# Optimization experiments

Measured on AMD Instinct MI355X. Metric: run time of the kernel, lower is better.

## Reference

```python
import jax, jax.numpy as jnp
import numpy as np

MS = [1, 2, 4, 8, 16]          # args.ms_token_size
RESI = 0.5                     # Phi resi_ratio
# PhiPartiallyShared: 4 phis, ticks = linspace(1/(2*4)... wait K==4 -> linspace(1/3/K, 1-1/3/K, K)
_TICKS = np.linspace(1.0 / 3.0 / 4.0, 1.0 - 1.0 / 3.0 / 4.0, 4)
PHI_IDX = [int(np.argmin(np.abs(_TICKS - (si / (len(MS) - 1))))) for si in range(len(MS))]


def _phi(h, w, b):
    # Phi.forward: h*(1-r) + conv3x3(h)*r
    c = jax.lax.conv_general_dilated(h, w, (1, 1), 'SAME',
                                     dimension_numbers=('NCHW', 'OIHW', 'NCHW'))
    c = c + b[None, :, None, None]
    return h * (1.0 - RESI) + c * RESI


def _area_down(z, ph, pw):
    # F.interpolate mode='area' with integer ratio == block mean
    B, C, H, W = z.shape
    return z.reshape(B, C, ph, H // ph, pw, W // pw).mean(axis=(3, 5))


def setup_inputs() -> dict:
    key = jax.random.key(0)
    k1, k2, k3 = jax.random.split(key, 3)
    B, C, H, W = 32, 64, 16, 16
    K = 8192
    f = jax.random.normal(k1, (B, C, H, W), dtype=jnp.float32)
    # nn.Embedding init: uniform(-1/K, 1/K)
    emb_w = jax.random.uniform(k2, (K, C), dtype=jnp.float32,
                               minval=-1.0 / K, maxval=1.0 / K)
    phi_w = jax.random.normal(k3, (4, C, C, 3, 3), dtype=jnp.float32) * 0.02
    phi_b = jnp.zeros((4, C), dtype=jnp.float32)
    return {'f': f, 'emb_w': emb_w, 'phi_w': phi_w, 'phi_b': phi_b}


def reference(f, emb_w, phi_w, phi_b):
    B, C, H, W = f.shape
    f = jax.lax.stop_gradient(f)  # z_enc.detach()
    z_rest = f
    f_hat = jnp.zeros_like(f)
    w_sq = jnp.sum(emb_w * emb_w, axis=1)  # [K]
    for si, pn in enumerate(MS):
        last = (si == len(MS) - 1)
        z = z_rest if last else _area_down(z_rest, pn, pn)
        zf = z.transpose(0, 2, 3, 1).reshape(-1, C)  # [B*pn*pn, C]
        # ||z||^2 + ||w||^2 - 2 z.w  (matches square-sum + addmm)
        d = jnp.sum(zf * zf, axis=1, keepdims=True) + w_sq[None, :] \
            - 2.0 * (zf @ emb_w.T)
        tok = jnp.argmin(d, axis=1)                  # [B*pn*pn]
        h = emb_w[tok].reshape(B, pn, pn, C).transpose(0, 3, 1, 2)
        if not last:
            h = jax.image.resize(h, (B, C, H, W), method='cubic')
        h = _phi(h, phi_w[PHI_IDX[si]], phi_b[PHI_IDX[si]])
        f_hat = f_hat + h
        z_rest = z_rest - h
    return f_hat
```

## Files before the change

### kernel.cpp

```cpp
#include <hip/hip_runtime.h>
#include <math.h>
#include <float.h>

#define BB 32
#define CC 64
#define KK 8192
#define NPIX 256
#define NELEM (BB*CC*NPIX)

typedef unsigned short u16;
typedef __attribute__((ext_vector_type(8))) short bf16x8;
typedef __attribute__((ext_vector_type(4))) float f32x4;

__device__ __forceinline__ u16 f2bf(float v) {
  unsigned u = __float_as_uint(v);
  return (u16)((u + 0x7FFFu + ((u >> 16) & 1u)) >> 16);
}

__global__ void k_prep(const float* __restrict__ f, float* __restrict__ zr,
                       float* __restrict__ out, const float* __restrict__ emb,
                       float* __restrict__ wsq32, u16* __restrict__ ehi) {
  int i = blockIdx.x * 256 + threadIdx.x;
  if (i < NELEM) { zr[i] = f[i]; out[i] = 0.f; ehi[i] = f2bf(emb[i]); }
  if (i < KK) {
    const float* row = emb + i * 64;
    double s = 0.0;
    #pragma unroll
    for (int c = 0; c < 64; ++c) s += (double)row[c] * (double)row[c];
    wsq32[i] = (float)s;
  }
}

__global__ void k_down(const float* __restrict__ zr, float* __restrict__ zd, int pn) {
#pragma clang fp contract(off)
  int i = blockIdx.x * 256 + threadIdx.x;
  int pnpn = pn * pn;
  int n = BB * CC * pnpn;
  if (i >= n) return;
  int x = i % pn; int y = (i / pn) % pn; int bc = i / pnpn;
  int bs = 16 / pn;
  const float* src = zr + bc * NPIX + (y * bs) * 16 + x * bs;
  float acc = 0.f;
  for (int dy = 0; dy < bs; ++dy) {
    const float* a = src + dy * 16;
    float s;
    if (bs == 16) {
      float r[8];
      #pragma unroll
      for (int j = 0; j < 8; ++j) r[j] = a[j] + a[8 + j];
      s = ((r[0] + r[1]) + (r[2] + r[3])) + ((r[4] + r[5]) + (r[6] + r[7]));
    } else if (bs == 8) {
      s = ((a[0] + a[1]) + (a[2] + a[3])) + ((a[4] + a[5]) + (a[6] + a[7]));
    } else if (bs == 4) {
      s = ((a[0] + a[1]) + a[2]) + a[3];
    } else {
      s = a[0] + a[1];
    }
    acc = acc + s;
  }
  zd[i] = acc * (1.f / (bs * bs));
}

__global__ __launch_bounds__(256) void k_pack(
    const float* __restrict__ zr, int pn, int bs,
    u16* __restrict__ zhi, float* __restrict__ zt32, float* __restrict__ zsq32) {
#pragma clang fp contract(off)
  int tid = threadIdx.x;
  int lv = tid >> 6, c = tid & 63;
  int vec = blockIdx.x * 4 + lv;
  int pnpn = pn * pn;
  int b = vec / pnpn, p = vec % pnpn;
  int y = p / pn, x = p % pn;
  const float* src = zr + ((size_t)(b * 64 + c)) * 256 + (y * bs) * 16 + x * bs;
  float v;
  if (bs == 1) {
    v = src[0];
  } else {
    v = (src[0] + src[1]) + (src[16] + src[17]);
    v = v * 0.25f;
  }
  zhi[(size_t)vec * 64 + c] = f2bf(v);
  zt32[(size_t)vec * 64 + c] = v;
  double sq = (double)v * (double)v;
  #pragma unroll
  for (int m = 1; m < 64; m <<= 1)
    sq += __shfl_xor(sq, m, 64);
  if (c == 0) zsq32[vec] = (float)sq;
}

__global__ __launch_bounds__(256, 4) void k_argmin(
    const float* __restrict__ zd, const float* __restrict__ emb,
    const float* __restrict__ wsq32,
    float* __restrict__ pd, int* __restrict__ pi,
    int numVec, int pnpn, int kchunk) {
#pragma clang fp contract(off)
  __shared__ __align__(16) float zt[32][68];
  __shared__ __align__(16) float et[64 * 64];
  __shared__ float ws_s[64];
  __shared__ float red_d[256];
  __shared__ int   red_i[256];
  int tid = threadIdx.x;
  int v0 = blockIdx.x * 32;
  int kbase = blockIdx.y * kchunk;

  for (int idx = tid; idx < 32 * 64; idx += 256) {
    int v = idx >> 6, c = idx & 63;
    int vi = v0 + v;
    float val = 0.f;
    if (vi < numVec) {
      int b = vi / pnpn, p = vi % pnpn;
      val = zd[(b * 64 + c) * pnpn + p];
    }
    zt[v][c] = val;
  }
  __syncthreads();

  const int v = tid & 31, kg = tid >> 5;
  float4 z4[16];
  #pragma unroll
  for (int i = 0; i < 16; ++i) z4[i] = *reinterpret_cast<float4*>(&zt[v][i * 4]);
  float zsq = 0.f;
  #pragma unroll
  for (int i = 0; i < 16; ++i)
    zsq += z4[i].x * z4[i].x + z4[i].y * z4[i].y + z4[i].z * z4[i].z + z4[i].w * z4[i].w;

  float bd = FLT_MAX; int bi = 0x7fffffff;
  for (int k0 = 0; k0 < kchunk; k0 += 64) {
    __syncthreads();
    {
      const float4* gsrc = reinterpret_cast<const float4*>(emb + (size_t)(kbase + k0) * 64);
      float4* ldst = reinterpret_cast<float4*>(et);
      #pragma unroll
      for (int idx = 0; idx < 4; ++idx)
        ldst[tid + idx * 256] = gsrc[tid + idx * 256];
    }
    if (tid < 64) ws_s[tid] = wsq32[kbase + k0 + tid];
    __syncthreads();
    #pragma unroll
    for (int j = 0; j < 8; ++j) {
      int kl = kg * 8 + j;
      const float4* e4 = reinterpret_cast<const float4*>(&et[kl * 64]);
      float acc = 0.f;
      #pragma unroll
      for (int i = 0; i < 16; ++i) {
        float4 e = e4[i];
        acc = __builtin_fmaf(z4[i].x, e.x, acc);
        acc = __builtin_fmaf(z4[i].y, e.y, acc);
        acc = __builtin_fmaf(z4[i].z, e.z, acc);
        acc = __builtin_fmaf(z4[i].w, e.w, acc);
      }
      float t1 = zsq + ws_s[kl];
      float d  = t1 - 2.0f * acc;
      if (d < bd) { bd = d; bi = kbase + k0 + kl; }
    }
  }
  red_d[tid] = bd; red_i[tid] = bi;
  __syncthreads();
  if (tid < 32) {
    float fb = red_d[tid]; int fi = red_i[tid];
    #pragma unroll
    for (int g = 1; g < 8; ++g) {
      float cd = red_d[g * 32 + tid]; int ci = red_i[g * 32 + tid];
      if (cd < fb || (cd == fb && ci < fi)) { fb = cd; fi = ci; }
    }
    int vi = v0 + tid;
    if (vi < numVec) {
      pd[blockIdx.y * numVec + vi] = fb;
      pi[blockIdx.y * numVec + vi] = fi;
    }
  }
}

#define INS4(dd, ii)                                                   \
  { bool c0 = (dd) < q0, c1 = (dd) < q1, c2 = (dd) < q2, c3 = (dd) < q3; \
    q3 = c2 ? q2 : (c3 ? (dd) : q3); j3 = c2 ? j2 : (c3 ? (ii) : j3);  \
    q2 = c1 ? q1 : (c2 ? (dd) : q2); j2 = c1 ? j1 : (c2 ? (ii) : j2);  \
    q1 = c0 ? q0 : (c1 ? (dd) : q1); j1 = c0 ? j0 : (c1 ? (ii) : j1);  \
    q0 = c0 ? (dd) : q0;             j0 = c0 ? (ii) : j0; }

__global__ __launch_bounds__(256, 4) void k_argmin_mfma(
    const u16* __restrict__ zhi, const float* __restrict__ zsq32,
    const u16* __restrict__ ehi, const float* __restrict__ wsq32,
    float* __restrict__ cdp, int* __restrict__ cip,
    int numVec, int part) {
  __shared__ u16  es[2][64 * 72];
  __shared__ float wss[2][64];
  const int tid = threadIdx.x;
  const int wid = tid >> 6, lane = tid & 63;
  const int l15 = lane & 15, l4 = lane >> 4;
  const int vw = blockIdx.x * 128 + wid * 32;
  const int kbase = blockIdx.y * part;
  const int KSx = gridDim.y;

  bf16x8 za[2][2];
  f32x4 zq[2];
  #pragma unroll
  for (int s = 0; s < 2; ++s) {
    const u16* zp = zhi + (size_t)(vw + s * 16 + l15) * 64 + l4 * 8;
    za[s][0] = *reinterpret_cast<const bf16x8*>(zp);
    za[s][1] = *reinterpret_cast<const bf16x8*>(zp + 32);
    zq[s] = *reinterpret_cast<const f32x4*>(zsq32 + vw + s * 16 + l4 * 4);
  }

  float d1[2][4], d2[2][4];
  int   i1[2][4], i2[2][4];
  #pragma unroll
  for (int s = 0; s < 2; ++s)
    #pragma unroll
    for (int r = 0; r < 4; ++r) {
      d1[s][r] = FLT_MAX; d2[s][r] = FLT_MAX;
      i1[s][r] = 0x7fffffff; i2[s][r] = 0x7fffffff;
    }

  const int NT = part >> 6;
  #define STAGE(buf, t)                                                      \
    { const u16* src = ehi + (size_t)(kbase + (t) * 64) * 64;                \
      int code = tid >> 2, seg = tid & 3;                                    \
      const bf16x8* s8 = reinterpret_cast<const bf16x8*>(src + code * 64 + seg * 16); \
      bf16x8 v0 = s8[0], v1 = s8[1];                                         \
      bf16x8* d8 = reinterpret_cast<bf16x8*>(&es[buf][code * 72 + seg * 16]);\
      d8[0] = v0; d8[1] = v1;                                                \
      if (tid < 64) wss[buf][tid] = wsq32[kbase + (t) * 64 + tid]; }

  STAGE(0, 0);
  __syncthreads();
  for (int t = 0; t < NT; ++t) {
    int cur = t & 1;
    if (t + 1 < NT) { STAGE(cur ^ 1, t + 1); }
    #pragma unroll
    for (int ct = 0; ct < 4; ++ct) {
      const u16* eb = &es[cur][(ct * 16 + l15) * 72 + l4 * 8];
      bf16x8 b0 = *reinterpret_cast<const bf16x8*>(eb);
      bf16x8 b1 = *reinterpret_cast<const bf16x8*>(eb + 32);
      float wl = wss[cur][ct * 16 + l15];
      int ki = kbase + t * 64 + ct * 16 + l15;
      #pragma unroll
      for (int s = 0; s < 2; ++s) {
        f32x4 acc = {0.f, 0.f, 0.f, 0.f};
        acc = __builtin_amdgcn_mfma_f32_16x16x32_bf16(za[s][0], b0, acc, 0, 0, 0);
        acc = __builtin_amdgcn_mfma_f32_16x16x32_bf16(za[s][1], b1, acc, 0, 0, 0);
        #pragma unroll
        for (int r = 0; r < 4; ++r) {
          float dd = __builtin_fmaf(acc[r], -2.f, wl);
          bool c0 = dd < d1[s][r];
          bool c1 = dd < d2[s][r];
          d2[s][r] = c0 ? d1[s][r] : (c1 ? dd : d2[s][r]);
          i2[s][r] = c0 ? i1[s][r] : (c1 ? ki : i2[s][r]);
          d1[s][r] = c0 ? dd : d1[s][r];
          i1[s][r] = c0 ? ki : i1[s][r];
        }
      }
    }
    __syncthreads();
  }

  #pragma unroll
  for (int s = 0; s < 2; ++s)
    #pragma unroll
    for (int r = 0; r < 4; ++r) {
      float q0 = d1[s][r], q1 = d2[s][r], q2 = FLT_MAX, q3 = FLT_MAX;
      int   j0 = i1[s][r], j1 = i2[s][r], j2 = 0x7fffffff, j3 = 0x7fffffff;
      #pragma unroll
      for (int m = 1; m < 16; m <<= 1) {
        float p0 = __shfl_xor(q0, m), p1 = __shfl_xor(q1, m);
        float p2 = __shfl_xor(q2, m), p3 = __shfl_xor(q3, m);
        int   o0 = __shfl_xor(j0, m), o1 = __shfl_xor(j1, m);
        int   o2 = __shfl_xor(j2, m), o3 = __shfl_xor(j3, m);
        INS4(p0, o0); INS4(p1, o1); INS4(p2, o2); INS4(p3, o3);
      }
      if (l15 == 0) {
        int vec = vw + s * 16 + l4 * 4 + r;
        float zqv = zq[s][r];
        size_t base = ((size_t)vec * KSx + blockIdx.y) * 4;
        cdp[base + 0] = zqv + q0; cdp[base + 1] = zqv + q1;
        cdp[base + 2] = zqv + q2; cdp[base + 3] = zqv + q3;
        cip[base + 0] = j0; cip[base + 1] = j1; cip[base + 2] = j2; cip[base + 3] = j3;
      }
    }
}

__global__ __launch_bounds__(256) void k_rescore(
    const float* __restrict__ cdp, const int* __restrict__ cip,
    const float* __restrict__ zt32, const float* __restrict__ emb,
    const float* __restrict__ wsq32, const float* __restrict__ zsq32,
    float* __restrict__ pd, int* __restrict__ pi,
    int numVec, int ncand) {
#pragma clang fp contract(off)
  __shared__ float zsh[4][64];
  int tid = threadIdx.x;
  int wid = tid >> 6, lane = tid & 63;
  int v0 = blockIdx.x * 4;
  zsh[wid][lane] = zt32[(size_t)v0 * 64 + tid];
  __syncthreads();

  int vec = v0 + wid;
  float zsq = zsq32[vec];
  const float* cdb = cdp + (size_t)vec * ncand;
  const int*   cib = cip + (size_t)vec * ncand;
  float dv0 = cdb[lane]; int ki0 = cib[lane];
  float dv1 = FLT_MAX;   int ki1 = 0x7fffffff;
  if (ncand > 64) { dv1 = cdb[lane + 64]; ki1 = cib[lane + 64]; }

  float dmin = fminf(dv0, dv1);
  #pragma unroll
  for (int m = 1; m < 64; m <<= 1) dmin = fminf(dmin, __shfl_xor(dmin, m, 64));
  float band = dmin + fmaf(sqrtf(zsq), 1.25e-5f, 1e-4f);

  const float* zw = zsh[wid];
  float d = FLT_MAX; int bi = 0x7fffffff;
  #pragma unroll
  for (int slot = 0; slot < 2; ++slot) {
    float dv = slot ? dv1 : dv0;
    int   kk = slot ? ki1 : ki0;
    if (dv <= band) {
      const float4* er = reinterpret_cast<const float4*>(emb + (size_t)kk * 64);
      float4 e4[16];
      #pragma unroll
      for (int i = 0; i < 16; ++i) e4[i] = er[i];
      float acc = 0.f;
      #pragma unroll
      for (int i = 0; i < 16; ++i) {
        acc = __builtin_fmaf(zw[4 * i + 0], e4[i].x, acc);
        acc = __builtin_fmaf(zw[4 * i + 1], e4[i].y, acc);
        acc = __builtin_fmaf(zw[4 * i + 2], e4[i].z, acc);
        acc = __builtin_fmaf(zw[4 * i + 3], e4[i].w, acc);
      }
      float t1 = zsq + wsq32[kk];
      float dd = t1 - 2.0f * acc;
      if (dd < d || (dd == d && kk < bi)) { d = dd; bi = kk; }
    }
  }
  #pragma unroll
  for (int m = 1; m < 64; m <<= 1) {
    float od = __shfl_xor(d, m, 64);
    int   oi = __shfl_xor(bi, m, 64);
    if (od < d || (od == d && oi < bi)) { d = od; bi = oi; }
  }
  if (lane == 0) { pd[vec] = 0.f; pi[vec] = bi; }
}

__global__ __launch_bounds__(256) void k_up(
    const float* __restrict__ pd, const int* __restrict__ pi,
    const float* __restrict__ emb, float* __restrict__ hup,
    int pn, int ksplit) {
  __shared__ float td[256];
  __shared__ int   ti[256];
  __shared__ int   tok_s[256];
  __shared__ float wsh[16][4];
  __shared__ int   i0sh[16];

  int t = threadIdx.x;
  int i = blockIdx.x * 256 + t;
  int p = i & 255; int c = (i >> 8) & 63; int b = i >> 14;
  int P = pn * pn;
  int numVec = BB * P;
  int R = 256 / P;
  int v = t % P, sg = t / P;

  float bd = FLT_MAX; int bi = 0x7fffffff;
  for (int s = sg; s < ksplit; s += R) {
    float cd = pd[s * numVec + b * P + v]; int ci = pi[s * numVec + b * P + v];
    if (cd < bd || (cd == bd && ci < bi)) { bd = cd; bi = ci; }
  }
  td[t] = bd; ti[t] = bi;
  __syncthreads();
  for (int r = R >> 1; r >= 1; r >>= 1) {
    if (sg < r) {
      float cd = td[t + r * P]; int ci = ti[t + r * P];
      if (cd < td[t] || (cd == td[t] && ci < ti[t])) { td[t] = cd; ti[t] = ci; }
    }
    __syncthreads();
  }
  if (t < P) tok_s[t] = ti[t];
  if (pn < 16 && t < 16) {
    double s = (t + 0.5) * ((double)pn / 16.0) - 0.5;
    int i0 = (int)floor(s) - 1;
    int hi = pn - 4; if (hi < 0) hi = 0;
    if (i0 < 0) i0 = 0; if (i0 > hi) i0 = hi;
    double wv[4]; double sum = 0.0;
    #pragma unroll
    for (int qq = 0; qq < 4; ++qq) {
      int ii = i0 + qq;
      double w = 0.0;
      if (ii < pn) {
        double xx = fabs(s - (double)ii);
        if (xx < 1.0)       w = ((1.5 * xx - 2.5) * xx) * xx + 1.0;
        else if (xx < 2.0)  w = ((-0.5 * xx + 2.5) * xx - 4.0) * xx + 2.0;
      }
      wv[qq] = w; sum += w;
    }
    i0sh[t] = i0;
    #pragma unroll
    for (int qq = 0; qq < 4; ++qq) wsh[t][qq] = (float)(wv[qq] / sum);
  }
  __syncthreads();

  if (pn == 16) { hup[i] = emb[(size_t)tok_s[p] * 64 + c]; return; }

  int y = p >> 4, x = p & 15;
  int iy0 = i0sh[y], ix0 = i0sh[x];
  float acc = 0.f;
  #pragma unroll
  for (int ty = 0; ty < 4; ++ty) {
    float wy = wsh[y][ty];
    int iy = iy0 + ty; if (iy > pn - 1) iy = pn - 1;
    float tmp = 0.f;
    #pragma unroll
    for (int tx = 0; tx < 4; ++tx) {
      float wx = wsh[x][tx];
      int ix = ix0 + tx; if (ix > pn - 1) ix = pn - 1;
      tmp += wx * emb[(size_t)tok_s[iy * pn + ix] * 64 + c];
    }
    acc += wy * tmp;
  }
  hup[i] = acc;
}

__global__ __launch_bounds__(256) void k_conv(
    const float* __restrict__ hup, const float* __restrict__ w,
    const float* __restrict__ bias, float* __restrict__ out, float* __restrict__ zr) {
  __shared__ __align__(16) float ins[16][18 * 18];
  __shared__ __align__(16) float wsh[8 * 64 * 12];
  int tid = threadIdx.x;
  int b = blockIdx.x;
  int ocb = blockIdx.y;

  for (int idx = tid; idx < 16 * 324; idx += 256)
    (&ins[0][0])[idx] = 0.f;
  for (int idx = tid; idx < 8 * 64 * 9; idx += 256) {
    int ocic = idx / 9, t = idx - ocic * 9;
    wsh[ocic * 12 + t] = w[(size_t)ocb * 8 * 64 * 9 + idx];
  }

  const int wid = tid >> 6, lane = tid & 63;
  const int ocg = wid >> 1;
  const int ph = (wid & 1) * 64 + lane;
  const int x = ph & 15, y2 = ph >> 4;

  float acc[4][2];
  #pragma unroll
  for (int j = 0; j < 4; ++j) {
    float bv = bias[ocb * 8 + ocg * 4 + j];
    acc[j][0] = bv; acc[j][1] = bv;
  }

  const float* hb = hup + (size_t)b * 64 * NPIX;
  float sreg[16];
  #pragma unroll
  for (int r = 0; r < 16; ++r) sreg[r] = hb[r * 256 + tid];

  for (int cc = 0; cc < 4; ++cc) {
    __syncthreads();
    #pragma unroll
    for (int r = 0; r < 16; ++r) {
      int idx = r * 256 + tid;
      int icl = idx >> 8, p = idx & 255;
      ins[icl][((p >> 4) + 1) * 18 + (p & 15) + 1] = sreg[r];
    }
    __syncthreads();
    if (cc < 3) {
      #pragma unroll
      for (int r = 0; r < 16; ++r) sreg[r] = hb[(cc + 1) * 4096 + r * 256 + tid];
    }

    #pragma unroll 2
    for (int icl = 0; icl < 16; ++icl) {
      float vt[4][3];
      const float* ip = &ins[icl][y2 * 2 * 18 + x];
      #pragma unroll
      for (int r = 0; r < 4; ++r)
        #pragma unroll
        for (int cxx = 0; cxx < 3; ++cxx)
          vt[r][cxx] = ip[r * 18 + cxx];

      int ic = cc * 16 + icl;
      #pragma unroll
      for (int j = 0; j < 4; ++j) {
        const float* wp = &wsh[((ocg * 4 + j) * 64 + ic) * 12];
        float4 wa = *reinterpret_cast<const float4*>(wp);
        float4 wb = *reinterpret_cast<const float4*>(wp + 4);
        float w8 = wp[8];
        float wv[9] = {wa.x, wa.y, wa.z, wa.w, wb.x, wb.y, wb.z, wb.w, w8};
        float a0 = acc[j][0], a1 = acc[j][1];
        #pragma unroll
        for (int dy = 0; dy < 3; ++dy)
          #pragma unroll
          for (int dx = 0; dx < 3; ++dx) {
            float wt = wv[dy * 3 + dx];
            a0 = __builtin_fmaf(vt[dy][dx], wt, a0);
            a1 = __builtin_fmaf(vt[dy + 1][dx], wt, a1);
          }
        acc[j][0] = a0; acc[j][1] = a1;
      }
    }
  }

  #pragma unroll
  for (int j = 0; j < 4; ++j) {
    int oc = ocb * 8 + ocg * 4 + j;
    #pragma unroll
    for (int r = 0; r < 2; ++r) {
      size_t gi = ((size_t)b * 64 + oc) * NPIX + (y2 * 2 + r) * 16 + x;
      float h = hup[gi];
      float ho = 0.5f * h + 0.5f * acc[j][r];
      out[gi] += ho;
      zr[gi]  -= ho;
    }
  }
}

extern "C" void kernel_launch(void* const* d_in, const int* in_sizes, int n_in,
                              void* d_out, int out_size, void* d_ws, size_t ws_size,
                              hipStream_t stream) {
  const float* f    = (const float*)d_in[0];
  const float* emb  = (const float*)d_in[1];
  const float* phiw = (const float*)d_in[2];
  const float* phib = (const float*)d_in[3];
  float* out = (float*)d_out;

  float* ws  = (float*)d_ws;
  float* zr     = ws;
  float* zd     = ws + 524288;
  float* hup    = ws + 557056;
  float* wsq32  = ws + 1081344;
  float* pd     = ws + 1089536;
  int*   pi     = (int*)(ws + 1097728);
  u16*   zhi    = (u16*)(ws + 1105920);
  u16*   ehi    = (u16*)(ws + 1368064);
  float* cand_d = ws + 1630208;
  int*   cand_i = (int*)(ws + 2154496);
  float* zsq32  = ws + 2678784;
  float* zt32   = ws + 2686976;

  double start = 1.0 / 3.0 / 4.0;
  double stop  = 1.0 - 1.0 / 3.0 / 4.0;
  double step  = (stop - start) / 3.0;
  double ticks[4] = { start, 1.0 * step + start, 2.0 * step + start, stop };
  int phi_idx[5];
  for (int si = 0; si < 5; ++si) {
    double xx = si / 4.0;
    int bj = 0; double bdd = fabs(ticks[0] - xx);
    for (int j = 1; j < 4; ++j) { double dd = fabs(ticks[j] - xx); if (dd < bdd) { bdd = dd; bj = j; } }
    phi_idx[si] = bj;
  }

  static const int MSarr[5] = {1, 2, 4, 8, 16};

  k_prep<<<NELEM / 256, 256, 0, stream>>>(f, zr, out, emb, wsq32, ehi);

  const int KS[5] = {128, 32, 16, 32, 16};
  for (int si = 0; si < 5; ++si) {
    int pn = MSarr[si], pnpn = pn * pn, numVec = BB * pnpn;
    int ksplit = KS[si];
    if (si >= 3) {
      int bs = 16 / pn;
      int part = KK / ksplit;
      k_pack<<<numVec / 4, 256, 0, stream>>>(zr, pn, bs, zhi, zt32, zsq32);
      dim3 g(numVec / 128, ksplit);
      k_argmin_mfma<<<g, 256, 0, stream>>>(zhi, zsq32, ehi, wsq32,
                                           cand_d, cand_i, numVec, part);
      k_rescore<<<numVec / 4, 256, 0, stream>>>(cand_d, cand_i, zt32, emb,
                                                wsq32, zsq32, pd, pi,
                                                numVec, ksplit * 4);
      k_up<<<NELEM / 256, 256, 0, stream>>>(pd, pi, emb, hup, pn, 1);
    } else {
      int n = BB * CC * pnpn;
      k_down<<<(n + 255) / 256, 256, 0, stream>>>(zr, zd, pn);
      int kchunk = KK / ksplit;
      dim3 g((numVec + 31) / 32, ksplit);
      k_argmin<<<g, 256, 0, stream>>>(zd, emb, wsq32, pd, pi, numVec, pnpn, kchunk);
      k_up<<<NELEM / 256, 256, 0, stream>>>(pd, pi, emb, hup, pn, ksplit);
    }
    int pidx = phi_idx[si];
    k_conv<<<dim3(BB, 8), 256, 0, stream>>>(hup, phiw + pidx * 64 * 64 * 9,
                                            phib + pidx * 64, out, zr);
  }
}
```

Baseline: 331.9 us.

## Pack candidate index into distance low bits for branchless top-2 selection

The MFMA argmin kernel now stores the local codebook index in the low 8 mantissa bits of each distance. That lets the running top-2 be kept with fmin and fmed3 instead of paired compare/select on separate index registers, and removes index shuffles and the index candidate buffer. The rescore kernel rebuilds global indices from the candidate slot position and the packed bits. The ||z||^2 term is dropped from the candidates, since only relative distances matter in the band test. Launch bounds rise to 8 blocks per CU and the last scale's K-split doubles so each partition stays within 256 codes, which trades lower register pressure for truncated distance precision that the rescore band must absorb.

```diff
diff --git a/kernel.cpp b/kernel.cpp
--- a/kernel.cpp
+++ b/kernel.cpp
@@ -171,17 +171,16 @@
   }
 }
 
-#define INS4(dd, ii)                                                   \
-  { bool c0 = (dd) < q0, c1 = (dd) < q1, c2 = (dd) < q2, c3 = (dd) < q3; \
-    q3 = c2 ? q2 : (c3 ? (dd) : q3); j3 = c2 ? j2 : (c3 ? (ii) : j3);  \
-    q2 = c1 ? q1 : (c2 ? (dd) : q2); j2 = c1 ? j1 : (c2 ? (ii) : j2);  \
-    q1 = c0 ? q0 : (c1 ? (dd) : q1); j1 = c0 ? j0 : (c1 ? (ii) : j1);  \
-    q0 = c0 ? (dd) : q0;             j0 = c0 ? (ii) : j0; }
-
-__global__ __launch_bounds__(256, 4) void k_argmin_mfma(
-    const u16* __restrict__ zhi, const float* __restrict__ zsq32,
-    const u16* __restrict__ ehi, const float* __restrict__ wsq32,
-    float* __restrict__ cdp, int* __restrict__ cip,
+#define INSK(kk)                                                       \
+  { bool c0 = (kk) < q0, c1 = (kk) < q1, c2 = (kk) < q2, c3 = (kk) < q3; \
+    q3 = c2 ? q2 : (c3 ? (kk) : q3);                                   \
+    q2 = c1 ? q1 : (c2 ? (kk) : q2);                                   \
+    q1 = c0 ? q0 : (c1 ? (kk) : q1);                                   \
+    q0 = c0 ? (kk) : q0; }
+
+__global__ __launch_bounds__(256, 8) void k_argmin_mfma(
+    const u16* __restrict__ zhi, const u16* __restrict__ ehi,
+    const float* __restrict__ wsq32, float* __restrict__ cdp,
     int numVec, int part) {
   __shared__ u16  es[2][64 * 72];
   __shared__ float wss[2][64];
@@ -193,24 +192,18 @@
   const int KSx = gridDim.y;
 
   bf16x8 za[2][2];
-  f32x4 zq[2];
   #pragma unroll
   for (int s = 0; s < 2; ++s) {
     const u16* zp = zhi + (size_t)(vw + s * 16 + l15) * 64 + l4 * 8;
     za[s][0] = *reinterpret_cast<const bf16x8*>(zp);
     za[s][1] = *reinterpret_cast<const bf16x8*>(zp + 32);
-    zq[s] = *reinterpret_cast<const f32x4*>(zsq32 + vw + s * 16 + l4 * 4);
   }
 
   float d1[2][4], d2[2][4];
-  int   i1[2][4], i2[2][4];
   #pragma unroll
   for (int s = 0; s < 2; ++s)
     #pragma unroll
-    for (int r = 0; r < 4; ++r) {
-      d1[s][r] = FLT_MAX; d2[s][r] = FLT_MAX;
-      i1[s][r] = 0x7fffffff; i2[s][r] = 0x7fffffff;
-    }
+    for (int r = 0; r < 4; ++r) { d1[s][r] = FLT_MAX; d2[s][r] = FLT_MAX; }
 
   const int NT = part >> 6;
   #define STAGE(buf, t)                                                      \
@@ -233,7 +226,7 @@
       bf16x8 b0 = *reinterpret_cast<const bf16x8*>(eb);
       bf16x8 b1 = *reinterpret_cast<const bf16x8*>(eb + 32);
       float wl = wss[cur][ct * 16 + l15];
-      int ki = kbase + t * 64 + ct * 16 + l15;
+      unsigned idu = (unsigned)(t * 64 + ct * 16 + l15);
       #pragma unroll
       for (int s = 0; s < 2; ++s) {
         f32x4 acc = {0.f, 0.f, 0.f, 0.f};
@@ -242,12 +235,10 @@
         #pragma unroll
         for (int r = 0; r < 4; ++r) {
           float dd = __builtin_fmaf(acc[r], -2.f, wl);
-          bool c0 = dd < d1[s][r];
-          bool c1 = dd < d2[s][r];
-          d2[s][r] = c0 ? d1[s][r] : (c1 ? dd : d2[s][r]);
-          i2[s][r] = c0 ? i1[s][r] : (c1 ? ki : i2[s][r]);
-          d1[s][r] = c0 ? dd : d1[s][r];
-          i1[s][r] = c0 ? ki : i1[s][r];
+          float key = __uint_as_float((__float_as_uint(dd) & 0xFFFFFF00u) | idu);
+          float o1 = d1[s][r];
+          d2[s][r] = __builtin_amdgcn_fmed3f(o1, key, d2[s][r]);
+          d1[s][r] = fminf(o1, key);
         }
       }
     }
@@ -259,30 +250,25 @@
     #pragma unroll
     for (int r = 0; r < 4; ++r) {
       float q0 = d1[s][r], q1 = d2[s][r], q2 = FLT_MAX, q3 = FLT_MAX;
-      int   j0 = i1[s][r], j1 = i2[s][r], j2 = 0x7fffffff, j3 = 0x7fffffff;
       #pragma unroll
       for (int m = 1; m < 16; m <<= 1) {
         float p0 = __shfl_xor(q0, m), p1 = __shfl_xor(q1, m);
         float p2 = __shfl_xor(q2, m), p3 = __shfl_xor(q3, m);
-        int   o0 = __shfl_xor(j0, m), o1 = __shfl_xor(j1, m);
-        int   o2 = __shfl_xor(j2, m), o3 = __shfl_xor(j3, m);
-        INS4(p0, o0); INS4(p1, o1); INS4(p2, o2); INS4(p3, o3);
+        INSK(p0); INSK(p1); INSK(p2); INSK(p3);
       }
       if (l15 == 0) {
         int vec = vw + s * 16 + l4 * 4 + r;
-        float zqv = zq[s][r];
         size_t base = ((size_t)vec * KSx + blockIdx.y) * 4;
-        cdp[base + 0] = zqv + q0; cdp[base + 1] = zqv + q1;
-        cdp[base + 2] = zqv + q2; cdp[base + 3] = zqv + q3;
-        cip[base + 0] = j0; cip[base + 1] = j1; cip[base + 2] = j2; cip[base + 3] = j3;
+        cdp[base + 0] = q0; cdp[base + 1] = q1;
+        cdp[base + 2] = q2; cdp[base + 3] = q3;
       }
     }
 }
 
 __global__ __launch_bounds__(256) void k_rescore(
-    const float* __restrict__ cdp, const int* __restrict__ cip,
-    const float* __restrict__ zt32, const float* __restrict__ emb,
-    const float* __restrict__ wsq32, const float* __restrict__ zsq32,
+    const float* __restrict__ cdp, const float* __restrict__ zt32,
+    const float* __restrict__ emb, const float* __restrict__ wsq32,
+    const float* __restrict__ zsq32,
     float* __restrict__ pd, int* __restrict__ pi,
     int numVec, int ncand) {
 #pragma clang fp contract(off)
@@ -296,10 +282,11 @@
   int vec = v0 + wid;
   float zsq = zsq32[vec];
   const float* cdb = cdp + (size_t)vec * ncand;
-  const int*   cib = cip + (size_t)vec * ncand;
-  float dv0 = cdb[lane]; int ki0 = cib[lane];
-  float dv1 = FLT_MAX;   int ki1 = 0x7fffffff;
-  if (ncand > 64) { dv1 = cdb[lane + 64]; ki1 = cib[lane + 64]; }
+  float dv0 = cdb[lane];
+  float dv1 = (ncand > 64) ? cdb[lane + 64] : FLT_MAX;
+  int j0 = lane, j1 = lane + 64;
+  int ki0 = ((j0 >> 2) << 8) | (int)(__float_as_uint(dv0) & 0xFFu);
+  int ki1 = ((j1 >> 2) << 8) | (int)(__float_as_uint(dv1) & 0xFFu);
 
   float dmin = fminf(dv0, dv1);
   #pragma unroll
@@ -528,7 +515,6 @@
   u16*   zhi    = (u16*)(ws + 1105920);
   u16*   ehi    = (u16*)(ws + 1368064);
   float* cand_d = ws + 1630208;
-  int*   cand_i = (int*)(ws + 2154496);
   float* zsq32  = ws + 2678784;
   float* zt32   = ws + 2686976;
 
@@ -548,7 +534,7 @@
 
   k_prep<<<NELEM / 256, 256, 0, stream>>>(f, zr, out, emb, wsq32, ehi);
 
-  const int KS[5] = {128, 32, 16, 32, 16};
+  const int KS[5] = {128, 32, 16, 32, 32};
   for (int si = 0; si < 5; ++si) {
     int pn = MSarr[si], pnpn = pn * pn, numVec = BB * pnpn;
     int ksplit = KS[si];
@@ -557,9 +543,8 @@
       int part = KK / ksplit;
       k_pack<<<numVec / 4, 256, 0, stream>>>(zr, pn, bs, zhi, zt32, zsq32);
       dim3 g(numVec / 128, ksplit);
-      k_argmin_mfma<<<g, 256, 0, stream>>>(zhi, zsq32, ehi, wsq32,
-                                           cand_d, cand_i, numVec, part);
-      k_rescore<<<numVec / 4, 256, 0, stream>>>(cand_d, cand_i, zt32, emb,
+      k_argmin_mfma<<<g, 256, 0, stream>>>(zhi, ehi, wsq32, cand_d, numVec, part);
+      k_rescore<<<numVec / 4, 256, 0, stream>>>(cand_d, zt32, emb,
                                                 wsq32, zsq32, pd, pi,
                                                 numVec, ksplit * 4);
       k_up<<<NELEM / 256, 256, 0, stream>>>(pd, pi, emb, hup, pn, 1);
```

New measurement: 326.0 us. Within noise of the previous version (-1.8%).
